# Kernel tuning notes

Hardware: AMD Instinct MI355X
Metric: run time of the kernel (lower is better)

Reference implementation:

```python
import jax, jax.numpy as jnp
import numpy as np

N_USERS = 50000
N_ITEMS = 4000
BATCH = 256
EPS = 1e-8


def setup_inputs() -> dict:
    key = jax.random.key(0)
    k1, k2 = jax.random.split(key)
    explicit_feedback = jax.random.uniform(k1, (N_USERS, N_ITEMS), dtype=jnp.float32)
    user_ids = jax.random.randint(k2, (BATCH,), 0, N_USERS, dtype=jnp.int64)
    return {"explicit_feedback": explicit_feedback, "user_ids": user_ids, "num_neighbors": 10}


def reference(explicit_feedback, user_ids, num_neighbors):
    F = explicit_feedback                              # [U, I]
    # norm = row-wise SUM OF SQUARES (no sqrt), as in the original module
    norm_all = jnp.maximum(jnp.sum(F * F, axis=1), EPS)          # [U]
    users = F[user_ids]                                          # [B, I]
    norm_users = jnp.maximum(jnp.sum(users * users, axis=1), EPS)  # [B]
    sim = (users @ F.T) / norm_users[:, None] / norm_all[None, :]  # [B, U]
    neighbor_sim, neighbor_idx = jax.lax.top_k(sim, num_neighbors)  # [B, k]
    weights = neighbor_sim / jnp.sum(neighbor_sim, axis=1, keepdims=True)  # [B, k]
    neighbors = F[neighbor_idx]                                   # [B, k, I]
    ratings = jnp.einsum("bk,bki->bi", weights, neighbors)        # [B, I]
    return ratings
```

## Files before the change

### kernel.cpp

```cpp
#include <hip/hip_runtime.h>
#include <hip/hip_bf16.h>

#define N_USERS 50000
#define N_ITEMS 4000
#define BATCH   256
#define KSTEPS  125
#define NWG     391
#define NEG_INF (-3.402823466e38f)

typedef __attribute__((ext_vector_type(8)))  __bf16 bfrag;
typedef __attribute__((ext_vector_type(16))) float  f32x16;

__device__ __forceinline__ unsigned short f2bf(float f) {
  unsigned u = __float_as_uint(f);
  return (unsigned short)((u + 0x7FFFu + ((u >> 16) & 1u)) >> 16);
}

__global__ __launch_bounds__(256) void prep_pack(
    const float* __restrict__ F, const int* __restrict__ uids,
    unsigned short* __restrict__ apack) {
  int m = blockIdx.x;
  const int f = m >> 5, lr = m & 31;
  size_t base = (size_t)uids[m] * N_ITEMS;
  for (int kk = threadIdx.x * 4; kk < N_ITEMS; kk += 1024) {
    float4 v = *(const float4*)(F + base + kk);
    ushort4 o;
    o.x = f2bf(v.x); o.y = f2bf(v.y); o.z = f2bf(v.z); o.w = f2bf(v.w);
    int idx = ((kk >> 4) * 8 + f) * 512 + (lr + ((kk >> 3) & 1) * 32) * 8 + (kk & 7);
    *(ushort4*)(apack + idx) = o;
  }
}

__global__ __launch_bounds__(256, 2) void gemm_topk(
    const float* __restrict__ F, const unsigned short* __restrict__ apack,
    float2* __restrict__ wstop) {
  union Smem {
    unsigned short Bs[2][128][40];
    float dump[256][33];
  };
  __shared__ Smem sm;
  __shared__ float norms[128];

  const int tid   = threadIdx.x;
  const int w     = tid >> 6, lane = tid & 63;
  const int lrow  = lane & 31, lhalf = lane >> 5;
  const int mh    = w >> 1, nh = w & 1;
  const int n0    = blockIdx.x * 128;

  const int brow = tid >> 1, bh = tid & 1;
  int grow = n0 + brow; if (grow >= N_USERS) grow = 0;
  const float4* bptr = (const float4*)(F + (size_t)grow * N_ITEMS) + bh * 4;
  const unsigned short* abase = apack + (mh * 4) * 512 + lane * 8;

  f32x16 acc[4][2];
  #pragma unroll
  for (int i = 0; i < 4; ++i)
    #pragma unroll
    for (int j = 0; j < 2; ++j)
      #pragma unroll
      for (int e = 0; e < 16; ++e) acc[i][j][e] = 0.f;

  float ssq = 0.f;
  float4 brA[4], brB[4];

#define LOADB(SET, T) do { \
    const float4* bp_ = bptr + (T) * 8; \
    _Pragma("unroll") for (int q_ = 0; q_ < 4; ++q_) SET[q_] = bp_[q_]; \
  } while (0)

#define CONVW(SET, BUF) do { \
    const float* vv_ = (const float*)SET; \
    union { unsigned short s[8]; uint4 v; } h0_, h1_; \
    _Pragma("unroll") for (int e_ = 0; e_ < 8; ++e_) h0_.s[e_] = f2bf(vv_[e_]); \
    _Pragma("unroll") for (int e_ = 0; e_ < 8; ++e_) h1_.s[e_] = f2bf(vv_[8 + e_]); \
    _Pragma("unroll") for (int e_ = 0; e_ < 16; ++e_) ssq = fmaf(vv_[e_], vv_[e_], ssq); \
    *(uint4*)&sm.Bs[BUF][brow][bh * 16]     = h0_.v; \
    *(uint4*)&sm.Bs[BUF][brow][bh * 16 + 8] = h1_.v; \
  } while (0)

#define STEP(T, CSET, LSET, PAR) do { \
    _Pragma("unroll") for (int s_ = 0; s_ < 2; ++s_) { \
      bfrag av_[4], bf_[2]; \
      _Pragma("unroll") for (int i_ = 0; i_ < 4; ++i_) \
        av_[i_] = *(const bfrag*)(abase + (T) * 8192 + s_ * 4096 + i_ * 512); \
      _Pragma("unroll") for (int jj_ = 0; jj_ < 2; ++jj_) \
        bf_[jj_] = *(const bfrag*)&sm.Bs[PAR][(2 * nh + jj_) * 32 + lrow][s_ * 16 + lhalf * 8]; \
      _Pragma("unroll") for (int i_ = 0; i_ < 4; ++i_) \
        _Pragma("unroll") for (int jj_ = 0; jj_ < 2; ++jj_) \
          acc[i_][jj_] = __builtin_amdgcn_mfma_f32_32x32x16_bf16(av_[i_], bf_[jj_], acc[i_][jj_], 0, 0, 0); \
    } \
    if ((T) + 2 < KSTEPS) LOADB(LSET, (T) + 2); \
    if ((T) + 1 < KSTEPS) CONVW(CSET, (PAR) ^ 1); \
    __syncthreads(); \
  } while (0)

  LOADB(brA, 0);
  LOADB(brB, 1);
  CONVW(brA, 0);
  __syncthreads();

  for (int t = 0; t < KSTEPS - 1; t += 2) {
    STEP(t,     brB, brA, 0);
    STEP(t + 1, brA, brB, 1);
  }
  STEP(KSTEPS - 1, brB, brA, 0);

#undef STEP
#undef CONVW
#undef LOADB

  ssq += __shfl_xor(ssq, 1);
  if (bh == 0) norms[brow] = fmaxf(ssq, 1e-8f);

  float tv[8]; int ti[8];
  #pragma unroll
  for (int q = 0; q < 8; ++q) { tv[q] = NEG_INF; ti[q] = 0; }

  #pragma unroll
  for (int p = 0; p < 4; ++p) {
    __syncthreads();
    if (nh == (p >> 1)) {
      const int jj  = p & 1;
      const int ugc = n0 + 32 * p + lrow;
      const float inv = 1.0f / norms[32 * p + lrow];
      #pragma unroll
      for (int i = 0; i < 4; ++i)
        #pragma unroll
        for (int r = 0; r < 16; ++r) {
          int mrow = 128 * mh + 32 * i + (r & 3) + 8 * (r >> 2) + 4 * lhalf;
          sm.dump[mrow][lrow] = (ugc < N_USERS) ? acc[i][jj][r] * inv : NEG_INF;
        }
    }
    __syncthreads();
    for (int c = 0; c < 32; ++c) {
      float v = sm.dump[tid][c];
      int ci = n0 + 32 * p + c;
      if (v > tv[7]) {
        #pragma unroll
        for (int q = 0; q < 8; ++q) {
          bool gt = v > tv[q];
          float ov = tv[q]; int oi = ti[q];
          tv[q] = gt ? v : ov; ti[q] = gt ? ci : oi;
          v = gt ? ov : v;     ci = gt ? oi : ci;
        }
      }
    }
  }

  float2* dst = wstop + ((size_t)blockIdx.x * 256 + tid) * 8;
  #pragma unroll
  for (int q = 0; q < 8; ++q) dst[q] = make_float2(tv[q], __int_as_float(ti[q]));
}

__global__ __launch_bounds__(64) void merge_topk(
    const float2* __restrict__ wstop, int* __restrict__ cand) {
  const int b = blockIdx.x, l = threadIdx.x;
  float tv[8]; int ti[8];
  #pragma unroll
  for (int q = 0; q < 8; ++q) { tv[q] = NEG_INF; ti[q] = 0; }
  for (int c = l; c < NWG * 8; c += 64) {
    int wg = c >> 3, q = c & 7;
    float2 e = wstop[((size_t)wg * 256 + b) * 8 + q];
    float v = e.x; int ci = __float_as_int(e.y);
    #pragma unroll
    for (int q2 = 0; q2 < 8; ++q2) {
      bool gt = v > tv[q2];
      float ov = tv[q2]; int oi = ti[q2];
      tv[q2] = gt ? v : ov; ti[q2] = gt ? ci : oi;
      v = gt ? ov : v;      ci = gt ? oi : ci;
    }
  }
  __shared__ float sv[512];
  __shared__ int   si[512];
  #pragma unroll
  for (int q = 0; q < 8; ++q) { sv[l * 8 + q] = tv[q]; si[l * 8 + q] = ti[q]; }
  __syncthreads();
  if (l == 0) {
    float bv[32]; int bi[32];
    #pragma unroll
    for (int q = 0; q < 32; ++q) { bv[q] = NEG_INF; bi[q] = 0; }
    for (int n = 0; n < 512; ++n) {
      float v = sv[n];
      if (v > bv[31]) {
        int ci = si[n];
        #pragma unroll
        for (int q = 0; q < 32; ++q) {
          bool gt = v > bv[q];
          float ov = bv[q]; int oi = bi[q];
          bv[q] = gt ? v : ov; bi[q] = gt ? ci : oi;
          v = gt ? ov : v;     ci = gt ? oi : ci;
        }
      }
    }
    #pragma unroll
    for (int q = 0; q < 32; ++q) cand[b * 32 + q] = bi[q];
  }
}

__global__ __launch_bounds__(64) void rescore(
    const float* __restrict__ F, const int* __restrict__ uids,
    const int* __restrict__ cand, double* __restrict__ simx) {
  const int pr = blockIdx.x;
  const int b  = pr >> 5;
  const int ci = cand[pr];
  const float* fa = F + (size_t)uids[b] * N_ITEMS;
  const float* fc = F + (size_t)ci * N_ITEMS;
  double dot = 0.0, ss = 0.0;
  for (int k = threadIdx.x * 4; k < N_ITEMS; k += 256) {
    float4 a = *(const float4*)(fa + k);
    float4 c = *(const float4*)(fc + k);
    dot += (double)a.x * c.x + (double)a.y * c.y + (double)a.z * c.z + (double)a.w * c.w;
    ss  += (double)c.x * c.x + (double)c.y * c.y + (double)c.z * c.z + (double)c.w * c.w;
  }
  #pragma unroll
  for (int off = 32; off > 0; off >>= 1) {
    dot += __shfl_down(dot, off);
    ss  += __shfl_down(ss, off);
  }
  if (threadIdx.x == 0) simx[pr] = dot / fmax(ss, 1e-8);
}

__global__ __launch_bounds__(256) void finalize(
    const float* __restrict__ F, const int* __restrict__ cand,
    const double* __restrict__ simx, float* __restrict__ out) {
  const int b = blockIdx.x;
  __shared__ float wsh[10];
  __shared__ int   ish[10];
  if (threadIdx.x == 0) {
    double bv[10]; int bi[10];
    #pragma unroll
    for (int q = 0; q < 10; ++q) { bv[q] = -1.0e300; bi[q] = 0; }
    for (int n = 0; n < 32; ++n) {
      double v = simx[b * 32 + n];
      int ci = cand[b * 32 + n];
      #pragma unroll
      for (int q = 0; q < 10; ++q) {
        bool gt = v > bv[q];
        double ov = bv[q]; int oi = bi[q];
        bv[q] = gt ? v : ov; bi[q] = gt ? ci : oi;
        v = gt ? ov : v;     ci = gt ? oi : ci;
      }
    }
    double s = 0.0;
    #pragma unroll
    for (int q = 0; q < 10; ++q) s += bv[q];
    #pragma unroll
    for (int q = 0; q < 10; ++q) { wsh[q] = (float)(bv[q] / s); ish[q] = bi[q]; }
  }
  __syncthreads();
  float wr[10]; size_t ro[10];
  #pragma unroll
  for (int q = 0; q < 10; ++q) { wr[q] = wsh[q]; ro[q] = (size_t)ish[q] * N_ITEMS; }
  for (int i = threadIdx.x; i < N_ITEMS; i += 256) {
    float a = 0.f;
    #pragma unroll
    for (int q = 0; q < 10; ++q) a = fmaf(wr[q], F[ro[q] + i], a);
    out[b * N_ITEMS + i] = a;
  }
}

extern "C" void kernel_launch(void* const* d_in, const int* in_sizes, int n_in,
                              void* d_out, int out_size, void* d_ws, size_t ws_size,
                              hipStream_t stream) {
  const float* F    = (const float*)d_in[0];
  const int*   uids = (const int*)d_in[1];
  float* out = (float*)d_out;
  char*  ws  = (char*)d_ws;

  unsigned short* apack = (unsigned short*)ws;
  float2* wstop = (float2*)(ws + 2097152);
  int*    cand  = (int*)(ws + 2097152 + 6406144);
  double* simx  = (double*)(ws + 2097152 + 6406144 + 32768);

  prep_pack<<<dim3(BATCH), dim3(256), 0, stream>>>(F, uids, apack);
  gemm_topk<<<dim3(NWG),   dim3(256), 0, stream>>>(F, apack, wstop);
  merge_topk<<<dim3(BATCH), dim3(64), 0, stream>>>(wstop, cand);
  rescore<<<dim3(BATCH * 32), dim3(64), 0, stream>>>(F, uids, cand, simx);
  finalize<<<dim3(BATCH), dim3(256), 0, stream>>>(F, cand, simx, out);
}
```

Before: 1.343 ms.

## Prefetch A fragments a step ahead, XOR-swizzle B LDS tile, use lighter barrier

The A operand fragments, which come from global memory, are now loaded into registers one K-step ahead into a double buffer, so their latency overlaps the MFMAs of the current step. The padded B shared tile (row stride 40) becomes an unpadded stride-32 layout with an XOR swizzle on both the write and read addresses, meant to avoid LDS bank conflicts while using less LDS. __syncthreads is replaced with an explicit lgkmcnt wait plus s_barrier, which does not wait on outstanding global loads. The extra A register buffers raise VGPR pressure, which could hurt occupancy under launch_bounds(256,2).

```diff
diff --git a/kernel.cpp b/kernel.cpp
--- a/kernel.cpp
+++ b/kernel.cpp
@@ -35,7 +35,7 @@
     const float* __restrict__ F, const unsigned short* __restrict__ apack,
     float2* __restrict__ wstop) {
   union Smem {
-    unsigned short Bs[2][128][40];
+    unsigned short Bs[2][128][32];
     float dump[256][33];
   };
   __shared__ Smem sm;
@@ -52,6 +52,22 @@
   const float4* bptr = (const float4*)(F + (size_t)grow * N_ITEMS) + bh * 4;
   const unsigned short* abase = apack + (mh * 4) * 512 + lane * 8;
 
+  unsigned short* bsbase = &sm.Bs[0][0][0];
+
+  const unsigned wsw   = ((unsigned)(brow & 7)) << 4;
+  const unsigned woff0 = ((unsigned)(brow * 64 + bh * 32))      ^ wsw;
+  const unsigned woff1 = ((unsigned)(brow * 64 + bh * 32 + 16)) ^ wsw;
+
+  unsigned roff[2][2];
+  #pragma unroll
+  for (int jj = 0; jj < 2; ++jj) {
+    int R = (2 * nh + jj) * 32 + lrow;
+    unsigned sw = ((unsigned)(R & 7)) << 4;
+    #pragma unroll
+    for (int s = 0; s < 2; ++s)
+      roff[jj][s] = ((unsigned)(R * 64 + s * 32 + lhalf * 16)) ^ sw;
+  }
+
   f32x16 acc[4][2];
   #pragma unroll
   for (int i = 0; i < 4; ++i)
@@ -62,52 +78,72 @@
 
   float ssq = 0.f;
   float4 brA[4], brB[4];
+  bfrag  avA[8], avB[8];
+
+#define LOADA(AV, T) do { \
+    _Pragma("unroll") for (int s_ = 0; s_ < 2; ++s_) \
+      _Pragma("unroll") for (int i_ = 0; i_ < 4; ++i_) \
+        AV[s_ * 4 + i_] = *(const bfrag*)(abase + (size_t)(T) * 8192 + s_ * 4096 + i_ * 512); \
+  } while (0)
 
 #define LOADB(SET, T) do { \
     const float4* bp_ = bptr + (T) * 8; \
     _Pragma("unroll") for (int q_ = 0; q_ < 4; ++q_) SET[q_] = bp_[q_]; \
   } while (0)
 
-#define CONVW(SET, BUF) do { \
+#define CONVW(SET, PAR) do { \
     const float* vv_ = (const float*)SET; \
-    union { unsigned short s[8]; uint4 v; } h0_, h1_; \
-    _Pragma("unroll") for (int e_ = 0; e_ < 8; ++e_) h0_.s[e_] = f2bf(vv_[e_]); \
-    _Pragma("unroll") for (int e_ = 0; e_ < 8; ++e_) h1_.s[e_] = f2bf(vv_[8 + e_]); \
+    union { unsigned short s_[8]; uint4 v_; } h0_, h1_; \
+    _Pragma("unroll") for (int e_ = 0; e_ < 8; ++e_) h0_.s_[e_] = f2bf(vv_[e_]); \
+    _Pragma("unroll") for (int e_ = 0; e_ < 8; ++e_) h1_.s_[e_] = f2bf(vv_[8 + e_]); \
     _Pragma("unroll") for (int e_ = 0; e_ < 16; ++e_) ssq = fmaf(vv_[e_], vv_[e_], ssq); \
-    *(uint4*)&sm.Bs[BUF][brow][bh * 16]     = h0_.v; \
-    *(uint4*)&sm.Bs[BUF][brow][bh * 16 + 8] = h1_.v; \
-  } while (0)
-
-#define STEP(T, CSET, LSET, PAR) do { \
+    char* wb_ = (char*)bsbase + (PAR) * 16384; \
+    *(uint4*)(wb_ + woff0) = h0_.v_; \
+    *(uint4*)(wb_ + woff1) = h1_.v_; \
+  } while (0)
+
+#define MFMA_STEP(AV, PAR) do { \
     _Pragma("unroll") for (int s_ = 0; s_ < 2; ++s_) { \
-      bfrag av_[4], bf_[2]; \
-      _Pragma("unroll") for (int i_ = 0; i_ < 4; ++i_) \
-        av_[i_] = *(const bfrag*)(abase + (T) * 8192 + s_ * 4096 + i_ * 512); \
+      bfrag bf_[2]; \
       _Pragma("unroll") for (int jj_ = 0; jj_ < 2; ++jj_) \
-        bf_[jj_] = *(const bfrag*)&sm.Bs[PAR][(2 * nh + jj_) * 32 + lrow][s_ * 16 + lhalf * 8]; \
+        bf_[jj_] = *(const bfrag*)((char*)bsbase + (PAR) * 16384 + roff[jj_][s_]); \
       _Pragma("unroll") for (int i_ = 0; i_ < 4; ++i_) \
         _Pragma("unroll") for (int jj_ = 0; jj_ < 2; ++jj_) \
-          acc[i_][jj_] = __builtin_amdgcn_mfma_f32_32x32x16_bf16(av_[i_], bf_[jj_], acc[i_][jj_], 0, 0, 0); \
+          acc[i_][jj_] = __builtin_amdgcn_mfma_f32_32x32x16_bf16(AV[s_ * 4 + i_], bf_[jj_], acc[i_][jj_], 0, 0, 0); \
     } \
+  } while (0)
+
+#define KBARRIER() do { \
+    asm volatile("s_waitcnt lgkmcnt(0)" ::: "memory"); \
+    __builtin_amdgcn_s_barrier(); \
+  } while (0)
+
+#define STEP(T, AVCUR, AVNXT, CSET, LSET, PAR) do { \
+    MFMA_STEP(AVCUR, PAR); \
+    if ((T) + 1 < KSTEPS) LOADA(AVNXT, (T) + 1); \
     if ((T) + 2 < KSTEPS) LOADB(LSET, (T) + 2); \
     if ((T) + 1 < KSTEPS) CONVW(CSET, (PAR) ^ 1); \
-    __syncthreads(); \
-  } while (0)
-
+    KBARRIER(); \
+  } while (0)
+
+  LOADA(avA, 0);
   LOADB(brA, 0);
   LOADB(brB, 1);
   CONVW(brA, 0);
-  __syncthreads();
+  KBARRIER();
 
   for (int t = 0; t < KSTEPS - 1; t += 2) {
-    STEP(t,     brB, brA, 0);
-    STEP(t + 1, brA, brB, 1);
-  }
-  STEP(KSTEPS - 1, brB, brA, 0);
+    STEP(t,     avA, avB, brB, brA, 0);
+    STEP(t + 1, avB, avA, brA, brB, 1);
+  }
+  STEP(KSTEPS - 1, avA, avB, brB, brA, 0);
 
 #undef STEP
+#undef KBARRIER
+#undef MFMA_STEP
 #undef CONVW
 #undef LOADB
+#undef LOADA
 
   ssq += __shfl_xor(ssq, 1);
   if (bh == 0) norms[brow] = fmaxf(ssq, 1e-8f);
```

New measurement: 1.290 ms. 3.9% less time.
